# Kernel optimization log

Measured on AMD Instinct MI355X. Metric: run time of the kernel, lower is better.

The kernel has to match this reference:

```python
import jax, jax.numpy as jnp
import numpy as np

N = 50000          # nodes
E_RAND = 600000    # random edges (self-loops appended -> E = 650000)
H, C = 2, 128      # heads, per-head channels
IN, OUT = 128, 40
SLOPE = 0.2        # PyG GATv2 default negative_slope
EPS = 1e-16


def setup_inputs() -> dict:
    key = jax.random.key(0)
    ks = jax.random.split(key, 16)
    x = jax.random.normal(ks[0], (N, IN), jnp.float32)
    src = jax.random.randint(ks[1], (E_RAND,), 0, N)
    dst = jax.random.randint(ks[2], (E_RAND,), 0, N)
    loops = jnp.arange(N)
    edge_index = jnp.stack([jnp.concatenate([src, loops]),
                            jnp.concatenate([dst, loops])]).astype(jnp.int64)

    def glorot(k, shape):
        fan = shape[0] + shape[-1]
        return jax.random.normal(k, shape, jnp.float32) * jnp.sqrt(2.0 / fan)

    return {
        "x": x, "edge_index": edge_index,
        "Wl1": glorot(ks[3], (IN, H * C)), "Wr1": glorot(ks[4], (IN, H * C)),
        "att1": glorot(ks[5], (H, C)), "b1": jnp.zeros((H * C,), jnp.float32),
        "Wl2": glorot(ks[6], (H * C, H * C)), "Wr2": glorot(ks[7], (H * C, H * C)),
        "att2": glorot(ks[8], (H, C)), "b2": jnp.zeros((H * C,), jnp.float32),
        "W3": glorot(ks[9], (H * C, C)), "b3": jnp.zeros((C,), jnp.float32),
        "W4": glorot(ks[10], (C, OUT)), "b4": jnp.zeros((OUT,), jnp.float32),
    }


def gatv2_conv(x, src, dst, Wl, Wr, att, b):
    # x: [N, F]; lin_l -> source messages, lin_r -> target. Output concat heads.
    xl = (x @ Wl).reshape(-1, H, C)              # [N,H,C]
    xr = (x @ Wr).reshape(-1, H, C)
    e = jax.nn.leaky_relu(xl[src] + xr[dst], SLOPE)   # [E,H,C]
    score = jnp.einsum('ehc,hc->eh', e, att)          # [E,H]
    # segment softmax over incoming edges of each dst node
    m = jax.ops.segment_max(score, dst, num_segments=N)       # [N,H]
    a = jnp.exp(score - m[dst])
    denom = jax.ops.segment_sum(a, dst, num_segments=N)
    alpha = a / (denom[dst] + EPS)                              # [E,H]
    out = jax.ops.segment_sum(alpha[:, :, None] * xl[src], dst, num_segments=N)
    return out.reshape(-1, H * C) + b


def reference(x, edge_index, Wl1, Wr1, att1, b1, Wl2, Wr2, att2, b2, W3, b3, W4, b4):
    src, dst = edge_index[0], edge_index[1]
    h = jax.nn.relu(gatv2_conv(x, src, dst, Wl1, Wr1, att1, b1))   # dropout: eval mode
    h = jax.nn.relu(gatv2_conv(h, src, dst, Wl2, Wr2, att2, b2))
    h = h @ W3 + b3
    h = h @ W4 + b4
    return jax.nn.sigmoid(h)   # [N, OUT]
```

## Files before the change

kernel.cpp:

```cpp
#include <hip/hip_runtime.h>
#include <hip/hip_bf16.h>
#include <math.h>

typedef __attribute__((ext_vector_type(4))) float f32x4;
typedef __attribute__((ext_vector_type(8))) short s16x8;
typedef __attribute__((ext_vector_type(8))) unsigned short u16x8;

#define CAP 48

__device__ inline unsigned short f2b(float f) {
    union { float f; unsigned u; } x; x.f = f;
    unsigned r = x.u + 0x7FFF + ((x.u >> 16) & 1);
    return (unsigned short)(r >> 16);
}
__device__ inline float b2f(unsigned short b) {
    union { unsigned u; float f; } x; x.u = ((unsigned)b) << 16; return x.f;
}

__device__ inline void gload_lds16(const void* g, void* l) {
    __builtin_amdgcn_global_load_lds(
        (const __attribute__((address_space(1))) void*)g,
        (__attribute__((address_space(3))) void*)l, 16, 0, 0);
}

#define GBM 128
#define GBN 256
#define GBK 64

__global__ __launch_bounds__(512) void gemm_mfma(
    const void* __restrict__ Aptr, const unsigned short* __restrict__ Bt,
    const float* __restrict__ bias, void* __restrict__ Cout, void* __restrict__ Cout2,
    int M, int Nn, int K, int split, int mode, int aflt)
{
    __shared__ unsigned short As[GBM * GBK];
    __shared__ unsigned short Bs[GBN * GBK];
    const int tid = threadIdx.x;
    const int lane = tid & 63;
    const int w = tid >> 6, wm = w >> 2, wn = w & 3;
    const int row0 = blockIdx.y * GBM, col0 = blockIdx.x * GBN;
    const int l15 = lane & 15, l7 = lane & 7, lhi = lane >> 4;

    f32x4 acc[4][4] = {};

    for (int k0 = 0; k0 < K; k0 += GBK) {
        if (aflt == 0) {
            const unsigned short* A = (const unsigned short*)Aptr;
            #pragma unroll
            for (int i = 0; i < 2; i++) {
                int L = i * 512 + tid;
                int row = L >> 3;
                int c = (L & 7) ^ (row & 7);
                int gr = row0 + row; gr = gr < M ? gr : M - 1;
                gload_lds16(A + (size_t)gr * K + k0 + c * 8, (char*)As + L * 16);
            }
        } else {
            const float* A = (const float*)Aptr;
            #pragma unroll
            for (int i = 0; i < 2; i++) {
                int L = i * 512 + tid;
                int row = L >> 3;
                int c = (L & 7) ^ (row & 7);
                int gr = row0 + row; gr = gr < M ? gr : M - 1;
                const float* ap = A + (size_t)gr * K + k0 + c * 8;
                float4 va = *(const float4*)ap;
                float4 vb = *(const float4*)(ap + 4);
                ushort4 o0 = { f2b(va.x), f2b(va.y), f2b(va.z), f2b(va.w) };
                ushort4 o1 = { f2b(vb.x), f2b(vb.y), f2b(vb.z), f2b(vb.w) };
                *(ushort4*)((char*)As + L * 16)     = o0;
                *(ushort4*)((char*)As + L * 16 + 8) = o1;
            }
        }
        #pragma unroll
        for (int i = 0; i < 4; i++) {
            int L = i * 512 + tid;
            int row = L >> 3;
            int c = (L & 7) ^ (row & 7);
            gload_lds16(Bt + (size_t)(col0 + row) * K + k0 + c * 8, (char*)Bs + L * 16);
        }
        __syncthreads();
        #pragma unroll
        for (int kk = 0; kk < 2; kk++) {
            s16x8 af[4], bf[4];
            #pragma unroll
            for (int i = 0; i < 4; i++) {
                int slot = (wm * 64 + i * 16 + l15) * 8 + ((kk * 4 + lhi) ^ l7);
                af[i] = *(const s16x8*)((const char*)As + slot * 16);
            }
            #pragma unroll
            for (int j = 0; j < 4; j++) {
                int slot = (wn * 64 + j * 16 + l15) * 8 + ((kk * 4 + lhi) ^ l7);
                bf[j] = *(const s16x8*)((const char*)Bs + slot * 16);
            }
            #pragma unroll
            for (int i = 0; i < 4; i++)
                #pragma unroll
                for (int j = 0; j < 4; j++)
                    acc[i][j] = __builtin_amdgcn_mfma_f32_16x16x32_bf16(
                        af[i], bf[j], acc[i][j], 0, 0, 0);
        }
        __syncthreads();
    }

    if (mode == 0) {
        unsigned short* C  = (unsigned short*)Cout;
        unsigned short* C2 = (unsigned short*)Cout2;
        const int ld2 = Nn - split;
        #pragma unroll
        for (int i = 0; i < 4; i++)
            #pragma unroll
            for (int r = 0; r < 4; r++) {
                int row = row0 + wm * 64 + i * 16 + lhi * 4 + r;
                if (row >= M) continue;
                #pragma unroll
                for (int j = 0; j < 4; j++) {
                    int col = col0 + wn * 64 + j * 16 + l15;
                    unsigned short val = f2b(acc[i][j][r]);
                    if (col < split) C[(size_t)row * split + col] = val;
                    else             C2[(size_t)row * ld2 + (col - split)] = val;
                }
            }
    } else {
        float* C = (float*)Cout;
        #pragma unroll
        for (int i = 0; i < 4; i++)
            #pragma unroll
            for (int r = 0; r < 4; r++) {
                int row = row0 + wm * 64 + i * 16 + lhi * 4 + r;
                if (row >= M) continue;
                #pragma unroll
                for (int j = 0; j < 4; j++) {
                    int col = col0 + wn * 64 + j * 16 + l15;
                    if (col >= split) continue;
                    float v = acc[i][j][r] + bias[col];
                    C[(size_t)row * split + col] = 1.f / (1.f + __expf(-v));
                }
            }
    }
}

#define PB 32
#define PC 96
#define PD 352
#define PEND 2892

__global__ __launch_bounds__(256) void k_prep(
    const float* __restrict__ Wl1, const float* __restrict__ Wr1,
    const float* __restrict__ Wl2, const float* __restrict__ Wr2,
    const float* __restrict__ W3,  const float* __restrict__ W4,
    const float* __restrict__ b3,  const float* __restrict__ b4,
    const int* __restrict__ src,   const int* __restrict__ dstv, int E,
    unsigned short* __restrict__ Wcat1, unsigned short* __restrict__ Wcat2,
    unsigned short* __restrict__ W34t, float* __restrict__ b34,
    int* __restrict__ cnt, int* __restrict__ colA)
{
    __shared__ float w4c[128];
    const int b = blockIdx.x, tid = threadIdx.x;

    if (b < PB) {
        int base = b * 2048 + tid * 8;
        #pragma unroll
        for (int j = 0; j < 8; j++) {
            int e = base + j;
            int ep = e & 32767, n = ep >> 7, k = ep & 127;
            const float* srcp = (e < 32768) ? Wl1 : Wr1;
            Wcat1[e] = f2b(srcp[k * 256 + n]);
        }
    } else if (b < PC) {
        int base = (b - PB) * 2048 + tid * 8;
        #pragma unroll
        for (int j = 0; j < 8; j++) {
            int e = base + j;
            int ep = e & 65535, n = ep >> 8, k = ep & 255;
            const float* srcp = (e < 65536) ? Wl2 : Wr2;
            Wcat2[e] = f2b(srcp[k * 256 + n]);
        }
    } else if (b < PD) {
        int n = b - PC;
        if (n < 40) {
            if (tid < 128) w4c[tid] = W4[tid * 40 + n];
            __syncthreads();
            float s = 0.f;
            const float4* p = (const float4*)&W3[(size_t)tid * 128];
            #pragma unroll
            for (int j = 0; j < 32; j++) {
                float4 v = p[j];
                s = fmaf(v.x, w4c[j * 4 + 0], s);
                s = fmaf(v.y, w4c[j * 4 + 1], s);
                s = fmaf(v.z, w4c[j * 4 + 2], s);
                s = fmaf(v.w, w4c[j * 4 + 3], s);
            }
            W34t[(size_t)n * 256 + tid] = f2b(s);
            if (tid == 0) {
                float t = b4[n];
                for (int j = 0; j < 128; j++) t = fmaf(b3[j], w4c[j], t);
                b34[n] = t;
            }
        } else {
            W34t[(size_t)n * 256 + tid] = 0;
        }
    } else {
        int e = (b - PD) * 256 + tid;
        if (e < E) {
            int d = dstv[e];
            int slot = atomicAdd(&cnt[d], 1);
            colA[d * CAP + slot] = src[e] << 8;
        }
    }
}

__global__ __launch_bounds__(256) void k_attn(const unsigned short* __restrict__ xl,
    const unsigned short* __restrict__ xr, const float* __restrict__ att,
    const int* __restrict__ cnt, const int* __restrict__ colA,
    const float* __restrict__ bias, int Nn, unsigned short* __restrict__ outp)
{
    int n = blockIdx.x * 4 + (threadIdx.x >> 6);
    int lane = threadIdx.x & 63;
    if (n >= Nn) return;
    const int lh = lane & 31;
    const int h  = lane >> 5;
    int r0 = n * CAP;
    int r1 = r0 + cnt[n];

    const float LOG2E = 1.4426950408889634f;
    u16x8 xb = *(const u16x8*)&xr[(size_t)n * 256 + lh * 8];
    float xrv[8], w[8];
    #pragma unroll
    for (int k = 0; k < 8; k++) { xrv[k] = b2f(xb[k]); w[k] = att[lh * 8 + k] * LOG2E; }

    float m = -INFINITY, l = 0.f;
    float acc[8] = {};

    auto update = [&](const u16x8& vb) {
        float v[8];
        #pragma unroll
        for (int k = 0; k < 8; k++) v[k] = b2f(vb[k]);
        float dot = 0.f;
        #pragma unroll
        for (int k = 0; k < 8; k++) {
            float t = v[k] + xrv[k];
            t = fmaxf(t, 0.2f * t);
            dot = fmaf(t, w[k], dot);
        }
        #pragma unroll
        for (int off = 1; off <= 8; off <<= 1) dot += __shfl_xor(dot, off);
        if (__ballot(dot > m + 8.f)) {
            float mn = fmaxf(m, dot);
            float sc = exp2f(m - mn);
            float we = exp2f(dot - mn);
            l = l * sc + we;
            #pragma unroll
            for (int k = 0; k < 8; k++) acc[k] = acc[k] * sc + we * v[k];
            m = mn;
        } else {
            float we = exp2f(dot - m);
            l += we;
            #pragma unroll
            for (int k = 0; k < 8; k++) acc[k] = fmaf(we, v[k], acc[k]);
        }
    };

    int s = r0 + h;
    for (; s + 2 < r1; s += 4) {
        int c0 = colA[s], c1 = colA[s + 2];
        u16x8 v0 = *(const u16x8*)&xl[(size_t)c0 + lh * 8];
        u16x8 v1 = *(const u16x8*)&xl[(size_t)c1 + lh * 8];
        update(v0);
        update(v1);
    }
    for (; s < r1; s += 2) {
        int c = colA[s];
        u16x8 v = *(const u16x8*)&xl[(size_t)c + lh * 8];
        update(v);
    }

    float mq = (m == -INFINITY) ? -1e30f : m;
    float mo = __shfl_xor(mq, 32);
    float lo = __shfl_xor(l, 32);
    float ms = fmaxf(mq, mo);
    float es = exp2f(mq - ms), eo = exp2f(mo - ms);
    float lt = l * es + lo * eo + 1e-16f;
    float inv = 1.f / lt;

    u16x8 o;
    #pragma unroll
    for (int k = 0; k < 8; k++) {
        float other = __shfl_xor(acc[k], 32);
        float r = (acc[k] * es + other * eo) * inv + bias[lh * 8 + k];
        o[k] = f2b(fmaxf(r, 0.f));
    }
    if (h == 0) *(u16x8*)&outp[(size_t)n * 256 + lh * 8] = o;
}

extern "C" void kernel_launch(void* const* d_in, const int* in_sizes, int n_in,
                              void* d_out, int out_size, void* d_ws, size_t ws_size,
                              hipStream_t stream)
{
    const float* x    = (const float*)d_in[0];
    const int*   ei   = (const int*)d_in[1];
    const float* Wl1  = (const float*)d_in[2];
    const float* Wr1  = (const float*)d_in[3];
    const float* att1 = (const float*)d_in[4];
    const float* b1   = (const float*)d_in[5];
    const float* Wl2  = (const float*)d_in[6];
    const float* Wr2  = (const float*)d_in[7];
    const float* att2 = (const float*)d_in[8];
    const float* b2   = (const float*)d_in[9];
    const float* W3   = (const float*)d_in[10];
    const float* b3   = (const float*)d_in[11];
    const float* W4   = (const float*)d_in[12];
    const float* b4   = (const float*)d_in[13];

    const int N = in_sizes[0] / 128;
    const int E = in_sizes[1] / 2;
    const int* src  = ei;
    const int* dstv = ei + E;
    float* out = (float*)d_out;

    char* ws = (char*)d_ws;
    size_t o = 0;
    auto alloc = [&](size_t bytes) -> void* {
        void* p = ws + o;
        o += (bytes + 255) & ~(size_t)255;
        return p;
    };
    unsigned short* Wcat1  = (unsigned short*)alloc(512 * 128 * 2);
    unsigned short* Wcat2  = (unsigned short*)alloc(512 * 256 * 2);
    unsigned short* W34t   = (unsigned short*)alloc(256 * 256 * 2);
    float*          b34    = (float*)alloc(128 * 4);
    unsigned short* xlb    = (unsigned short*)alloc((size_t)N * 256 * 2);
    unsigned short* xrb    = (unsigned short*)alloc((size_t)N * 256 * 2);
    unsigned short* h1b    = (unsigned short*)alloc((size_t)N * 256 * 2);
    unsigned short* h2b    = (unsigned short*)alloc((size_t)N * 256 * 2);
    int* cnt    = (int*)alloc((size_t)N * 4);
    int* colA   = (int*)alloc((size_t)N * CAP * 4);

    dim3 blk(256);

    hipMemsetAsync(cnt, 0, (size_t)N * 4, stream);
    k_prep<<<PEND, blk, 0, stream>>>(Wl1, Wr1, Wl2, Wr2, W3, W4, b3, b4,
                                     src, dstv, E, Wcat1, Wcat2, W34t, b34,
                                     cnt, colA);

    const int gy = (N + GBM - 1) / GBM;

    gemm_mfma<<<dim3(2, gy), dim3(512), 0, stream>>>(x, Wcat1, nullptr, xlb, xrb,
                                                     N, 512, 128, 256, 0, 1);
    k_attn<<<(N + 3) / 4, blk, 0, stream>>>(xlb, xrb, att1, cnt, colA, b1, N, h1b);

    gemm_mfma<<<dim3(2, gy), dim3(512), 0, stream>>>(h1b, Wcat2, nullptr, xlb, xrb,
                                                     N, 512, 256, 256, 0, 0);
    k_attn<<<(N + 3) / 4, blk, 0, stream>>>(xlb, xrb, att2, cnt, colA, b2, N, h2b);

    gemm_mfma<<<dim3(1, gy), dim3(512), 0, stream>>>(h2b, W34t, b34, out, nullptr,
                                                     N, 128, 256, 40, 2, 0);
}
```

Measured before the change: 252.5 us.

## Use full-width 128x512 GEMM tile so each A tile is loaded once

Adds a 1024-thread GEMM kernel whose tile covers all 512 output columns (xl and xr together), so each row block of A is read and, for the fp32 input, converted to bf16 only once instead of twice across two column blocks. The old GEMM is specialized to the final sigmoid layer only. The adjacency fill in prep now uses nontemporal stores. The bigger block uses 80KB of LDS and 1024 threads, which lowers occupancy and halves the number of blocks in the grid.

```diff
diff --git a/kernel.cpp b/kernel.cpp
--- a/kernel.cpp
+++ b/kernel.cpp
@@ -23,59 +23,131 @@
         (__attribute__((address_space(3))) void*)l, 16, 0, 0);
 }
 
+#define WBM 128
+#define WBN 512
+#define WBK 64
+
+__global__ __launch_bounds__(1024) void gemm_mfma_w(
+    const void* __restrict__ Aptr, const unsigned short* __restrict__ Bt,
+    void* __restrict__ Cout, void* __restrict__ Cout2,
+    int M, int K, int split, int aflt)
+{
+    __shared__ unsigned short As[WBM * WBK];
+    __shared__ unsigned short Bs[WBN * WBK];
+    const int tid = threadIdx.x;
+    const int lane = tid & 63;
+    const int w = tid >> 6, wm = w >> 3, wn = w & 7;
+    const int row0 = blockIdx.y * WBM;
+    const int l15 = lane & 15, l7 = lane & 7, lhi = lane >> 4;
+
+    f32x4 acc[4][4] = {};
+
+    for (int k0 = 0; k0 < K; k0 += WBK) {
+        if (aflt == 0) {
+            const unsigned short* A = (const unsigned short*)Aptr;
+            int L = tid;
+            int row = L >> 3;
+            int c = (L & 7) ^ (row & 7);
+            int gr = row0 + row; gr = gr < M ? gr : M - 1;
+            gload_lds16(A + (size_t)gr * K + k0 + c * 8, (char*)As + L * 16);
+        } else {
+            const float* A = (const float*)Aptr;
+            int L = tid;
+            int row = L >> 3;
+            int c = (L & 7) ^ (row & 7);
+            int gr = row0 + row; gr = gr < M ? gr : M - 1;
+            const float* ap = A + (size_t)gr * K + k0 + c * 8;
+            float4 va = *(const float4*)ap;
+            float4 vb = *(const float4*)(ap + 4);
+            ushort4 o0 = { f2b(va.x), f2b(va.y), f2b(va.z), f2b(va.w) };
+            ushort4 o1 = { f2b(vb.x), f2b(vb.y), f2b(vb.z), f2b(vb.w) };
+            *(ushort4*)((char*)As + L * 16)     = o0;
+            *(ushort4*)((char*)As + L * 16 + 8) = o1;
+        }
+        #pragma unroll
+        for (int i = 0; i < 4; i++) {
+            int L = i * 1024 + tid;
+            int row = L >> 3;
+            int c = (L & 7) ^ (row & 7);
+            gload_lds16(Bt + (size_t)row * K + k0 + c * 8, (char*)Bs + L * 16);
+        }
+        __syncthreads();
+        #pragma unroll
+        for (int kk = 0; kk < 2; kk++) {
+            s16x8 af[4], bf[4];
+            #pragma unroll
+            for (int i = 0; i < 4; i++) {
+                int slot = (wm * 64 + i * 16 + l15) * 8 + ((kk * 4 + lhi) ^ l7);
+                af[i] = *(const s16x8*)((const char*)As + slot * 16);
+            }
+            #pragma unroll
+            for (int j = 0; j < 4; j++) {
+                int slot = (wn * 64 + j * 16 + l15) * 8 + ((kk * 4 + lhi) ^ l7);
+                bf[j] = *(const s16x8*)((const char*)Bs + slot * 16);
+            }
+            #pragma unroll
+            for (int i = 0; i < 4; i++)
+                #pragma unroll
+                for (int j = 0; j < 4; j++)
+                    acc[i][j] = __builtin_amdgcn_mfma_f32_16x16x32_bf16(
+                        af[i], bf[j], acc[i][j], 0, 0, 0);
+        }
+        __syncthreads();
+    }
+
+    unsigned short* C  = (unsigned short*)Cout;
+    unsigned short* C2 = (unsigned short*)Cout2;
+    const int ld2 = WBN - split;
+    #pragma unroll
+    for (int i = 0; i < 4; i++)
+        #pragma unroll
+        for (int r = 0; r < 4; r++) {
+            int row = row0 + wm * 64 + i * 16 + lhi * 4 + r;
+            if (row >= M) continue;
+            #pragma unroll
+            for (int j = 0; j < 4; j++) {
+                int col = wn * 64 + j * 16 + l15;
+                unsigned short val = f2b(acc[i][j][r]);
+                if (col < split) C[(size_t)row * split + col] = val;
+                else             C2[(size_t)row * ld2 + (col - split)] = val;
+            }
+        }
+}
+
 #define GBM 128
 #define GBN 256
 #define GBK 64
 
 __global__ __launch_bounds__(512) void gemm_mfma(
-    const void* __restrict__ Aptr, const unsigned short* __restrict__ Bt,
-    const float* __restrict__ bias, void* __restrict__ Cout, void* __restrict__ Cout2,
-    int M, int Nn, int K, int split, int mode, int aflt)
+    const unsigned short* __restrict__ A, const unsigned short* __restrict__ Bt,
+    const float* __restrict__ bias, float* __restrict__ C,
+    int M, int K, int split)
 {
     __shared__ unsigned short As[GBM * GBK];
     __shared__ unsigned short Bs[GBN * GBK];
     const int tid = threadIdx.x;
     const int lane = tid & 63;
     const int w = tid >> 6, wm = w >> 2, wn = w & 3;
-    const int row0 = blockIdx.y * GBM, col0 = blockIdx.x * GBN;
+    const int row0 = blockIdx.y * GBM;
     const int l15 = lane & 15, l7 = lane & 7, lhi = lane >> 4;
 
     f32x4 acc[4][4] = {};
 
     for (int k0 = 0; k0 < K; k0 += GBK) {
-        if (aflt == 0) {
-            const unsigned short* A = (const unsigned short*)Aptr;
-            #pragma unroll
-            for (int i = 0; i < 2; i++) {
-                int L = i * 512 + tid;
-                int row = L >> 3;
-                int c = (L & 7) ^ (row & 7);
-                int gr = row0 + row; gr = gr < M ? gr : M - 1;
-                gload_lds16(A + (size_t)gr * K + k0 + c * 8, (char*)As + L * 16);
-            }
-        } else {
-            const float* A = (const float*)Aptr;
-            #pragma unroll
-            for (int i = 0; i < 2; i++) {
-                int L = i * 512 + tid;
-                int row = L >> 3;
-                int c = (L & 7) ^ (row & 7);
-                int gr = row0 + row; gr = gr < M ? gr : M - 1;
-                const float* ap = A + (size_t)gr * K + k0 + c * 8;
-                float4 va = *(const float4*)ap;
-                float4 vb = *(const float4*)(ap + 4);
-                ushort4 o0 = { f2b(va.x), f2b(va.y), f2b(va.z), f2b(va.w) };
-                ushort4 o1 = { f2b(vb.x), f2b(vb.y), f2b(vb.z), f2b(vb.w) };
-                *(ushort4*)((char*)As + L * 16)     = o0;
-                *(ushort4*)((char*)As + L * 16 + 8) = o1;
-            }
+        #pragma unroll
+        for (int i = 0; i < 2; i++) {
+            int L = i * 512 + tid;
+            int row = L >> 3;
+            int c = (L & 7) ^ (row & 7);
+            int gr = row0 + row; gr = gr < M ? gr : M - 1;
+            gload_lds16(A + (size_t)gr * K + k0 + c * 8, (char*)As + L * 16);
         }
         #pragma unroll
         for (int i = 0; i < 4; i++) {
             int L = i * 512 + tid;
             int row = L >> 3;
             int c = (L & 7) ^ (row & 7);
-            gload_lds16(Bt + (size_t)(col0 + row) * K + k0 + c * 8, (char*)Bs + L * 16);
+            gload_lds16(Bt + (size_t)row * K + k0 + c * 8, (char*)Bs + L * 16);
         }
         __syncthreads();
         #pragma unroll
@@ -101,41 +173,20 @@
         __syncthreads();
     }
 
-    if (mode == 0) {
-        unsigned short* C  = (unsigned short*)Cout;
-        unsigned short* C2 = (unsigned short*)Cout2;
-        const int ld2 = Nn - split;
-        #pragma unroll
-        for (int i = 0; i < 4; i++)
-            #pragma unroll
-            for (int r = 0; r < 4; r++) {
-                int row = row0 + wm * 64 + i * 16 + lhi * 4 + r;
-                if (row >= M) continue;
-                #pragma unroll
-                for (int j = 0; j < 4; j++) {
-                    int col = col0 + wn * 64 + j * 16 + l15;
-                    unsigned short val = f2b(acc[i][j][r]);
-                    if (col < split) C[(size_t)row * split + col] = val;
-                    else             C2[(size_t)row * ld2 + (col - split)] = val;
-                }
-            }
-    } else {
-        float* C = (float*)Cout;
-        #pragma unroll
-        for (int i = 0; i < 4; i++)
-            #pragma unroll
-            for (int r = 0; r < 4; r++) {
-                int row = row0 + wm * 64 + i * 16 + lhi * 4 + r;
-                if (row >= M) continue;
-                #pragma unroll
-                for (int j = 0; j < 4; j++) {
-                    int col = col0 + wn * 64 + j * 16 + l15;
-                    if (col >= split) continue;
-                    float v = acc[i][j][r] + bias[col];
-                    C[(size_t)row * split + col] = 1.f / (1.f + __expf(-v));
-                }
-            }
-    }
+    #pragma unroll
+    for (int i = 0; i < 4; i++)
+        #pragma unroll
+        for (int r = 0; r < 4; r++) {
+            int row = row0 + wm * 64 + i * 16 + lhi * 4 + r;
+            if (row >= M) continue;
+            #pragma unroll
+            for (int j = 0; j < 4; j++) {
+                int col = wn * 64 + j * 16 + l15;
+                if (col >= split) continue;
+                float v = acc[i][j][r] + bias[col];
+                C[(size_t)row * split + col] = 1.f / (1.f + __expf(-v));
+            }
+        }
 }
 
 #define PB 32
@@ -203,7 +254,7 @@
         if (e < E) {
             int d = dstv[e];
             int slot = atomicAdd(&cnt[d], 1);
-            colA[d * CAP + slot] = src[e] << 8;
+            __builtin_nontemporal_store(src[e] << 8, &colA[d * CAP + slot]);
         }
     }
 }
@@ -341,16 +392,16 @@
                                      src, dstv, E, Wcat1, Wcat2, W34t, b34,
                                      cnt, colA);
 
-    const int gy = (N + GBM - 1) / GBM;
-
-    gemm_mfma<<<dim3(2, gy), dim3(512), 0, stream>>>(x, Wcat1, nullptr, xlb, xrb,
-                                                     N, 512, 128, 256, 0, 1);
+    const int gy = (N + 127) / 128;
+
+    gemm_mfma_w<<<dim3(1, gy), dim3(1024), 0, stream>>>(x, Wcat1, xlb, xrb,
+                                                        N, 128, 256, 1);
     k_attn<<<(N + 3) / 4, blk, 0, stream>>>(xlb, xrb, att1, cnt, colA, b1, N, h1b);
 
-    gemm_mfma<<<dim3(2, gy), dim3(512), 0, stream>>>(h1b, Wcat2, nullptr, xlb, xrb,
-                                                     N, 512, 256, 256, 0, 0);
+    gemm_mfma_w<<<dim3(1, gy), dim3(1024), 0, stream>>>(h1b, Wcat2, xlb, xrb,
+                                                        N, 256, 256, 0);
     k_attn<<<(N + 3) / 4, blk, 0, stream>>>(xlb, xrb, att2, cnt, colA, b2, N, h2b);
 
-    gemm_mfma<<<dim3(1, gy), dim3(512), 0, stream>>>(h2b, W34t, b34, out, nullptr,
-                                                     N, 128, 256, 40, 2, 0);
-}
+    gemm_mfma<<<dim3(1, gy), dim3(512), 0, stream>>>(h2b, W34t, b34, out,
+                                                     N, 256, 40);
+}
```

New measurement: 262.9 us. 1.04x slower.
